# Performance work log

Measured on AMD Instinct MI355X. Metric: run time of the kernel, lower is better.

## Reference

```python
import jax, jax.numpy as jnp
import numpy as np

MARGIN = 1.0
N, D = 4096, 512
NUM_CLASSES = 64


def setup_inputs() -> dict:
    key = jax.random.key(0)
    k1, k2 = jax.random.split(key)
    inputs = jax.random.normal(k1, (N, D), dtype=jnp.float32)
    targets = jax.random.randint(k2, (N,), 0, NUM_CLASSES, dtype=jnp.int64)
    return {"inputs": inputs, "targets": targets}


def reference(inputs, targets):
    n = inputs.shape[0]
    sq = jnp.sum(inputs * inputs, axis=1)  # [n]
    # squared Euclidean distances, clamped at 0 (matches relu in original)
    d2 = jnp.maximum(sq[:, None] + sq[None, :] - 2.0 * (inputs @ inputs.T), 0.0)
    # safe sqrt (zero entries get 0, matching forward; avoids NaN grads)
    dist = jnp.where(d2 > 0, jnp.sqrt(jnp.where(d2 > 0, d2, 1.0)), 0.0)  # [n,n]

    same = targets[:, None] == targets[None, :]
    eye = jnp.eye(n, dtype=bool)
    pos_mask = same & ~eye          # positives, diagonal excluded
    neg_mask = ~same                # negatives (diagonal is same-label, excluded)

    # per-row sum_k exp(margin - d_ik) over negatives  (replaces per-pair loop)
    neg_sum = jnp.sum(jnp.where(neg_mask, jnp.exp(MARGIN - dist), 0.0), axis=1)  # [n]

    # J_ij = log(neg_sum_i + neg_sum_j) + d_ij for positive pairs
    J = jnp.log(neg_sum[:, None] + neg_sum[None, :]) + dist
    triu_pos = jnp.triu(pos_mask)   # loop iterated over upper-triangular positives
    hinge2 = jnp.where(triu_pos, jax.nn.relu(J) ** 2, 0.0)

    # original divides by count of ALL positive entries (both triangles)
    len_p = jnp.sum(pos_mask).astype(jnp.float32)
    return jnp.sum(hinge2) / len_p
```

## Files before the change

kernel.cpp:

```cpp
#include <hip/hip_runtime.h>
#include <math.h>

#define NN 4096
#define DD 512
#define MARGINF 1.0f
#define NCLS 64
#define MAXM 160
#define TRI (MAXM * (MAXM - 1) / 2)
#define NBLK 2080
#define NSLICE 4

typedef __attribute__((ext_vector_type(8))) short bf16x8;
typedef __attribute__((ext_vector_type(4))) float f32x4;

#define WS_SQ   0
#define WS_NS   4096
#define WS_LOSS 8192
#define WS_CTR  8193
#define WS_LENP 8194
#define WS_RK   8320
#define WS_MEM  12416
#define WS_XF   32768
#define WS_PD   1081344

__device__ __forceinline__ unsigned short f2bf(float f) {
    unsigned u = __float_as_uint(f);
    u += 0x7fffu + ((u >> 16) & 1u);
    return (unsigned short)(u >> 16);
}

__global__ __launch_bounds__(256) void prep_kernel(const float* __restrict__ X,
                                                   const int* __restrict__ tgt,
                                                   float* __restrict__ ws) {
    __shared__ int tg[NN];
    const int tid = threadIdx.x;
    for (int j = tid; j < NN; j += 256) tg[j] = tgt[j];

    const int wv = tid >> 6, lane = tid & 63;
    const int row = blockIdx.x * 4 + wv;
    const float4* xr = (const float4*)(X + (size_t)row * DD);
    float4 a = xr[2 * lane], b = xr[2 * lane + 1];
    float s = a.x * a.x + a.y * a.y + a.z * a.z + a.w * a.w
            + b.x * b.x + b.y * b.y + b.z * b.z + b.w * b.w;
#pragma unroll
    for (int off = 32; off; off >>= 1) s += __shfl_down(s, off, 64);

    ushort4 pa = {f2bf(a.x), f2bf(a.y), f2bf(a.z), f2bf(a.w)};
    ushort4 pb = {f2bf(b.x), f2bf(b.y), f2bf(b.z), f2bf(b.w)};
    const int r16 = row >> 4, m = row & 15;
    const int kb = lane >> 2, q = lane & 3;
    ushort4* dst = (ushort4*)((unsigned short*)(ws + WS_XF)
                              + ((size_t)(r16 * 16 + kb) * 64 + q * 16 + m) * 8);
    dst[0] = pa;
    dst[1] = pb;

    __syncthreads();
    const int myc = tg[row];
    int cnt = 0;
    for (int j = lane; j < row; j += 64) cnt += (tg[j] == myc) ? 1 : 0;
#pragma unroll
    for (int off = 32; off; off >>= 1) cnt += __shfl_down(cnt, off, 64);
    if (lane == 0) {
        ws[WS_SQ + row] = s;
        ws[WS_NS + row] = 0.0f;
        ((int*)(ws + WS_RK))[row] = cnt;
        if (cnt < MAXM) ((int*)(ws + WS_MEM))[myc * MAXM + cnt] = row;
    }
    if (blockIdx.x == 0 && tid == 0) {
        ws[WS_LOSS] = 0.0f;
        ((unsigned*)ws)[WS_CTR] = 0u;
        ws[WS_LENP] = 0.0f;
    }
}

__global__ __launch_bounds__(256, 6) void negsum_kernel(const int* __restrict__ tgt,
                                                        float* __restrict__ ws) {
    __shared__ unsigned short lds[3][8][512];
    const int bidx = (blockIdx.x & 7) * 260 + (blockIdx.x >> 3);
    int bj = (int)((sqrtf(8.0f * (float)bidx + 1.0f) - 1.0f) * 0.5f);
    while (bj * (bj + 1) / 2 > bidx) --bj;
    while ((bj + 1) * (bj + 2) / 2 <= bidx) ++bj;
    const int bi = bidx - bj * (bj + 1) / 2;
    const int i0 = bi * 64, j0 = bj * 64;

    const int tid = threadIdx.x;
    const int w = tid >> 6, lane = tid & 63;
    const int m_ = lane & 15, q = lane >> 4;
    const int wr = (w & 1) * 32, wc = (w >> 1) * 32;
    const unsigned short* Xf = (const unsigned short*)(ws + WS_XF);
    const int air0 = i0 >> 4, bjr0 = j0 >> 4;

    int fr16[2];
#pragma unroll
    for (int s = 0; s < 2; ++s) {
        const int f = w * 2 + s;
        fr16[s] = (f < 4) ? (air0 + f) : (bjr0 + (f - 4));
    }

#define DMA_CHUNK(kb_, buf_)                                                   \
    {                                                                          \
        _Pragma("unroll")                                                      \
        for (int s = 0; s < 2; ++s) {                                          \
            const unsigned short* gp =                                         \
                Xf + ((size_t)fr16[s] * 16 + (kb_)) * 512 + lane * 8;          \
            __builtin_amdgcn_global_load_lds(                                  \
                (const __attribute__((address_space(1))) int*)gp,              \
                (__attribute__((address_space(3))) int*)(&lds[buf_][w * 2 + s][0]), \
                16, 0, 0);                                                     \
        }                                                                      \
    }

    f32x4 acc[2][2] = {};

    DMA_CHUNK(0, 0)
    DMA_CHUNK(1, 1)
    asm volatile("s_waitcnt vmcnt(2)" ::: "memory");
    __builtin_amdgcn_s_barrier();

#pragma unroll
    for (int t = 0; t < 16; ++t) {
        const int cur = t % 3;
        if (t < 14) DMA_CHUNK(t + 2, (t + 2) % 3)
        bf16x8 af[2], bf[2];
#pragma unroll
        for (int u = 0; u < 2; ++u)
            af[u] = *(const bf16x8*)&lds[cur][(w & 1) * 2 + u][lane * 8];
#pragma unroll
        for (int v = 0; v < 2; ++v)
            bf[v] = *(const bf16x8*)&lds[cur][4 + (w >> 1) * 2 + v][lane * 8];
        acc[0][0] = __builtin_amdgcn_mfma_f32_16x16x32_bf16(af[0], bf[0], acc[0][0], 0, 0, 0);
        acc[0][1] = __builtin_amdgcn_mfma_f32_16x16x32_bf16(af[0], bf[1], acc[0][1], 0, 0, 0);
        acc[1][0] = __builtin_amdgcn_mfma_f32_16x16x32_bf16(af[1], bf[0], acc[1][0], 0, 0, 0);
        acc[1][1] = __builtin_amdgcn_mfma_f32_16x16x32_bf16(af[1], bf[1], acc[1][1], 0, 0, 0);
        if (t < 14) {
            asm volatile("s_waitcnt vmcnt(2)" ::: "memory");
            __builtin_amdgcn_s_barrier();
        } else if (t == 14) {
            asm volatile("s_waitcnt vmcnt(0)" ::: "memory");
            __builtin_amdgcn_s_barrier();
        }
    }
#undef DMA_CHUNK

    const float* sq = ws + WS_SQ;
    float* ns = ws + WS_NS;
    const int* rk = (const int*)(ws + WS_RK);
    float* posd = ws + WS_PD;
    float sjv[2]; int tjv[2], jv[2];
#pragma unroll
    for (int v = 0; v < 2; ++v) {
        int j = j0 + wc + v * 16 + m_;
        jv[v] = j;
        sjv[v] = sq[j];
        tjv[v] = tgt[j];
    }
    float colp[2] = {0.0f, 0.0f};
#pragma unroll
    for (int u = 0; u < 2; ++u) {
#pragma unroll
        for (int r = 0; r < 4; ++r) {
            const int i = i0 + wr + u * 16 + q * 4 + r;
            const float si = sq[i];
            const int ti = tgt[i];
            float rp = 0.0f;
#pragma unroll
            for (int v = 0; v < 2; ++v) {
                float d2 = si + sjv[v] - 2.0f * acc[u][v][r];
                float dist = d2 > 0.0f ? sqrtf(d2) : 0.0f;
                if (tjv[v] != ti) {
                    float e = __expf(MARGINF - dist);
                    rp += e;
                    colp[v] += e;
                } else if (i < jv[v]) {
                    int ra = rk[i], rb = rk[jv[v]];
                    if (ra < MAXM && rb < MAXM) {
                        int hi = ra > rb ? ra : rb;
                        int lo = ra > rb ? rb : ra;
                        posd[ti * TRI + hi * (hi - 1) / 2 + lo] = dist;
                    }
                }
            }
            rp += __shfl_xor(rp, 1, 64);
            rp += __shfl_xor(rp, 2, 64);
            rp += __shfl_xor(rp, 4, 64);
            rp += __shfl_xor(rp, 8, 64);
            if (m_ == 0) atomicAdd(&ns[i], rp);
        }
    }
    if (bi != bj) {
#pragma unroll
        for (int v = 0; v < 2; ++v) {
            float cp = colp[v];
            cp += __shfl_xor(cp, 16, 64);
            cp += __shfl_xor(cp, 32, 64);
            if (q == 0) atomicAdd(&ns[jv[v]], cp);
        }
    }
}

__global__ __launch_bounds__(256) void pair2_kernel(const int* __restrict__ tgt,
                                                    float* __restrict__ ws,
                                                    float* __restrict__ out) {
    __shared__ float wsum[4];
    __shared__ int csum[4];
    __shared__ bool last;
    const int c = blockIdx.x >> 2;
    const int sl = blockIdx.x & 3;
    const int tid = threadIdx.x;
    const int wv = tid >> 6, lane = tid & 63;

    int ccount = 0;
    for (int j = tid; j < NN; j += 256) ccount += (tgt[j] == c) ? 1 : 0;
#pragma unroll
    for (int off = 32; off; off >>= 1) ccount += __shfl_down(ccount, off, 64);
    if (lane == 0) csum[wv] = ccount;
    __syncthreads();
    int mc = csum[0] + csum[1] + csum[2] + csum[3];
    if (mc > MAXM) mc = MAXM;
    const int P = mc * (mc - 1) / 2;

    const int* mem = (const int*)(ws + WS_MEM) + c * MAXM;
    const float* pd = ws + WS_PD + c * TRI;
    const float* ns = ws + WS_NS;
    float lsum = 0.0f;
    for (int p = tid + sl * 256; p < P; p += 256 * NSLICE) {
        int b = (int)((1.0f + sqrtf(1.0f + 8.0f * (float)p)) * 0.5f);
        while (b * (b - 1) / 2 > p) --b;
        while ((b + 1) * b / 2 <= p) ++b;
        const int a = p - b * (b - 1) / 2;
        const float dist = pd[b * (b - 1) / 2 + a];
        const int i = mem[a], j = mem[b];
        float J = __logf(ns[i] + ns[j]) + dist;
        float h = fmaxf(J, 0.0f);
        lsum += h * h;
    }
#pragma unroll
    for (int off = 32; off; off >>= 1) lsum += __shfl_xor(lsum, off, 64);
    if (lane == 0) wsum[wv] = lsum;
    __syncthreads();
    if (tid == 0) {
        float s = wsum[0] + wsum[1] + wsum[2] + wsum[3];
        if (s != 0.0f) atomicAdd(&ws[WS_LOSS], s);
        if (sl == 0) atomicAdd(&ws[WS_LENP], (float)(mc * (mc - 1)));
        __threadfence();
        unsigned d = atomicAdd((unsigned*)ws + WS_CTR, 1u);
        last = (d == NCLS * NSLICE - 1);
    }
    __syncthreads();
    if (last && tid == 0) {
        float total = atomicAdd(&ws[WS_LOSS], 0.0f);
        float lp = atomicAdd(&ws[WS_LENP], 0.0f);
        out[0] = total / lp;
    }
}

extern "C" void kernel_launch(void* const* d_in, const int* in_sizes, int n_in,
                              void* d_out, int out_size, void* d_ws, size_t ws_size,
                              hipStream_t stream) {
    const float* X  = (const float*)d_in[0];
    const int*  tgt = (const int*)d_in[1];
    float* ws  = (float*)d_ws;
    float* out = (float*)d_out;

    hipLaunchKernelGGL(prep_kernel, dim3(NN / 4), dim3(256), 0, stream, X, tgt, ws);
    hipLaunchKernelGGL(negsum_kernel, dim3(NBLK), dim3(256), 0, stream, tgt, ws);
    hipLaunchKernelGGL(pair2_kernel, dim3(NCLS * NSLICE), dim3(256), 0, stream, tgt, ws, out);
}
```

Baseline: 107.8 us.

## Process two adjacent column tiles per block sharing the row-tile LDS loads

Each negsum block now covers one 64-row tile against two consecutive 64-column tiles using 512 threads. The row tile's bf16 chunks are DMA'd into LDS once and shared by both halves, cutting global loads and block count from 2080 to 1056. When the pair runs off the edge, the duplicated second tile is still computed and then discarded via early return. The risks are lower occupancy from larger blocks and more LDS, plus some wasted work on edge blocks.

```diff
diff --git a/kernel.cpp b/kernel.cpp
--- a/kernel.cpp
+++ b/kernel.cpp
@@ -7,7 +7,7 @@
 #define NCLS 64
 #define MAXM 160
 #define TRI (MAXM * (MAXM - 1) / 2)
-#define NBLK 2080
+#define NPAIR 1056
 #define NSLICE 4
 
 typedef __attribute__((ext_vector_type(8))) short bf16x8;
@@ -73,32 +73,40 @@
     }
 }
 
-__global__ __launch_bounds__(256, 6) void negsum_kernel(const int* __restrict__ tgt,
+__global__ __launch_bounds__(512, 8) void negsum_kernel(const int* __restrict__ tgt,
                                                         float* __restrict__ ws) {
-    __shared__ unsigned short lds[3][8][512];
-    const int bidx = (blockIdx.x & 7) * 260 + (blockIdx.x >> 3);
-    int bj = (int)((sqrtf(8.0f * (float)bidx + 1.0f) - 1.0f) * 0.5f);
-    while (bj * (bj + 1) / 2 > bidx) --bj;
-    while ((bj + 1) * (bj + 2) / 2 <= bidx) ++bj;
-    const int bi = bidx - bj * (bj + 1) / 2;
-    const int i0 = bi * 64, j0 = bj * 64;
+    __shared__ unsigned short lds[3][12][512];
+    const int sw = (blockIdx.x & 7) * 132 + (blockIdx.x >> 3);
+    int bi = 0, rem = sw;
+    while (true) {
+        const int s = (65 - bi) >> 1;
+        if (rem < s) break;
+        rem -= s; ++bi;
+    }
+    const int bj1 = bi + 2 * rem;
+    const bool has2 = (bj1 + 1) < 64;
+    const int bj2e = has2 ? bj1 + 1 : bj1;
+    const int i0 = bi * 64;
 
     const int tid = threadIdx.x;
     const int w = tid >> 6, lane = tid & 63;
     const int m_ = lane & 15, q = lane >> 4;
-    const int wr = (w & 1) * 32, wc = (w >> 1) * 32;
+    const int tsel = w >> 2, q2 = w & 3;
+    const int wr = (q2 & 1) * 32, wc = (q2 >> 1) * 32;
+    const int bjw = tsel ? bj2e : bj1;
+    const int j0w = bjw * 64;
     const unsigned short* Xf = (const unsigned short*)(ws + WS_XF);
-    const int air0 = i0 >> 4, bjr0 = j0 >> 4;
 
     int fr16[2];
 #pragma unroll
     for (int s = 0; s < 2; ++s) {
         const int f = w * 2 + s;
-        fr16[s] = (f < 4) ? (air0 + f) : (bjr0 + (f - 4));
+        fr16[s] = (f < 4) ? (bi * 4 + f)
+                          : ((f < 8) ? (bj1 * 4 + (f - 4)) : (bj2e * 4 + (f - 8)));
     }
 
 #define DMA_CHUNK(kb_, buf_)                                                   \
-    {                                                                          \
+    if (w < 6) {                                                               \
         _Pragma("unroll")                                                      \
         for (int s = 0; s < 2; ++s) {                                          \
             const unsigned short* gp =                                         \
@@ -124,10 +132,10 @@
         bf16x8 af[2], bf[2];
 #pragma unroll
         for (int u = 0; u < 2; ++u)
-            af[u] = *(const bf16x8*)&lds[cur][(w & 1) * 2 + u][lane * 8];
+            af[u] = *(const bf16x8*)&lds[cur][(q2 & 1) * 2 + u][lane * 8];
 #pragma unroll
         for (int v = 0; v < 2; ++v)
-            bf[v] = *(const bf16x8*)&lds[cur][4 + (w >> 1) * 2 + v][lane * 8];
+            bf[v] = *(const bf16x8*)&lds[cur][4 + tsel * 4 + (q2 >> 1) * 2 + v][lane * 8];
         acc[0][0] = __builtin_amdgcn_mfma_f32_16x16x32_bf16(af[0], bf[0], acc[0][0], 0, 0, 0);
         acc[0][1] = __builtin_amdgcn_mfma_f32_16x16x32_bf16(af[0], bf[1], acc[0][1], 0, 0, 0);
         acc[1][0] = __builtin_amdgcn_mfma_f32_16x16x32_bf16(af[1], bf[0], acc[1][0], 0, 0, 0);
@@ -142,6 +150,7 @@
     }
 #undef DMA_CHUNK
 
+    if (tsel == 1 && !has2) return;
     const float* sq = ws + WS_SQ;
     float* ns = ws + WS_NS;
     const int* rk = (const int*)(ws + WS_RK);
@@ -149,7 +158,7 @@
     float sjv[2]; int tjv[2], jv[2];
 #pragma unroll
     for (int v = 0; v < 2; ++v) {
-        int j = j0 + wc + v * 16 + m_;
+        int j = j0w + wc + v * 16 + m_;
         jv[v] = j;
         sjv[v] = sq[j];
         tjv[v] = tgt[j];
@@ -187,7 +196,7 @@
             if (m_ == 0) atomicAdd(&ns[i], rp);
         }
     }
-    if (bi != bj) {
+    if (bi != bjw) {
 #pragma unroll
         for (int v = 0; v < 2; ++v) {
             float cp = colp[v];
@@ -263,6 +272,6 @@
     float* out = (float*)d_out;
 
     hipLaunchKernelGGL(prep_kernel, dim3(NN / 4), dim3(256), 0, stream, X, tgt, ws);
-    hipLaunchKernelGGL(negsum_kernel, dim3(NBLK), dim3(256), 0, stream, tgt, ws);
+    hipLaunchKernelGGL(negsum_kernel, dim3(NPAIR), dim3(512), 0, stream, tgt, ws);
     hipLaunchKernelGGL(pair2_kernel, dim3(NCLS * NSLICE), dim3(256), 0, stream, tgt, ws, out);
 }
```

New measurement: 113.6 us. +5.4%, slower.
